# Kernel optimization log

Measured on AMD Instinct MI355X. Metric: run time of the kernel, lower is better.

Reference implementation:

```python
import jax, jax.numpy as jnp
import numpy as np

N_NODES = 100000
N_EDGES = 1000000
D_NODE = 64
D_EDGE = 32
D_OUT = 64
EPS = 1e-07
BETA = 1.0


def setup_inputs() -> dict:
    key = jax.random.key(0)
    ks = jax.random.split(key, 6)
    node_feats = jax.random.normal(ks[0], (N_NODES, D_NODE), dtype=jnp.float32)
    edge_feats = jax.random.normal(ks[1], (N_EDGES, D_EDGE), dtype=jnp.float32)
    src = jax.random.randint(ks[2], (N_EDGES,), 0, N_NODES, dtype=jnp.int32)
    dst = jax.random.randint(ks[3], (N_EDGES,), 0, N_NODES, dtype=jnp.int32)
    We = jax.random.normal(ks[4], (D_EDGE, D_OUT), dtype=jnp.float32) / np.sqrt(D_EDGE)
    be = jnp.zeros((D_OUT,), dtype=jnp.float32)
    Wm = jax.random.normal(ks[5], (D_NODE, D_OUT), dtype=jnp.float32) / np.sqrt(D_NODE)
    bm = jnp.zeros((D_OUT,), dtype=jnp.float32)
    return {"node_feats": node_feats, "edge_feats": edge_feats, "src": src,
            "dst": dst, "We": We, "be": be, "Wm": Wm, "bm": bm}


def reference(node_feats, edge_feats, src, dst, We, be, Wm, bm):
    n = node_feats.shape[0]
    # edge encoder + u_add_e: m_e = h_src + Linear(e)
    m = node_feats[src] + (edge_feats @ We + be)          # [E, D]
    m = jax.nn.relu(m) + EPS
    # segmented (per-destination) softmax over edges, per feature channel
    z = m * BETA
    zmax = jax.ops.segment_max(z, dst, num_segments=n)    # [N, D]
    ez = jnp.exp(z - zmax[dst])                           # [E, D]
    denom = jax.ops.segment_sum(ez, dst, num_segments=n)  # [N, D]
    a = ez / denom[dst]                                   # [E, D]
    # weighted scatter-sum aggregation
    agg = jax.ops.segment_sum(m * a, dst, num_segments=n) # [N, D]
    feats = node_feats + agg
    # mlp_layers=1 -> single Linear
    return feats @ Wm + bm
```

## Files before the change

kernel.cpp:

```cpp
#include <hip/hip_runtime.h>

#define D_NODE 64
#define D_EDGE 32
#define D_OUT  64
#define EPSF   1e-7f
#define CAP    48
#define CHUNK  8

typedef const __attribute__((address_space(1))) unsigned int guint_t;
typedef __attribute__((address_space(3))) unsigned int luint_t;

__global__ __launch_bounds__(256) void genconv_build_kernel(
    const int* __restrict__ src,
    const int* __restrict__ dst,
    int* __restrict__ cnt,
    int2* __restrict__ slots,
    int E)
{
    const int e = blockIdx.x * blockDim.x + threadIdx.x;
    if (e >= E) return;
    const int d = dst[e];
    const int pos = atomicAdd(&cnt[d], 1);
    if (pos < CAP)
        slots[d * CAP + pos] = make_int2(e, src[e]);
}

__global__ __launch_bounds__(256) void genconv_gather_kernel(
    const float* __restrict__ node,
    const float* __restrict__ ef,
    const int*  __restrict__ cnt,
    const int2* __restrict__ slots,
    const float* __restrict__ We,
    const float* __restrict__ be,
    const float* __restrict__ Wm,
    const float* __restrict__ bm,
    float* __restrict__ out,
    int N)
{
    __shared__ float wm_s[D_NODE * D_OUT];
    __shared__ __align__(16) float efs[4][2][CHUNK * D_EDGE];
    __shared__ __align__(16) float fbuf[4][D_NODE];

    for (int i = threadIdx.x; i < D_NODE * D_OUT; i += blockDim.x)
        wm_s[i] = Wm[i];
    __syncthreads();

    const int lane  = (int)(threadIdx.x & 63);
    const int wslot = (int)(threadIdx.x >> 6);
    float* const efA = efs[wslot][0];
    float* const efB = efs[wslot][1];

    float w[D_EDGE];
#pragma unroll
    for (int k = 0; k < D_EDGE; ++k)
        w[k] = We[k * D_OUT + lane];
    const float bias_e = be[lane];
    const float bias_m = bm[lane];

    const int wid = (int)((blockIdx.x * blockDim.x + threadIdx.x) >> 6);
    const int nw  = (int)((gridDim.x * blockDim.x) >> 6);

    int n = wid;
    int   c_pf   = 0;
    int2  sl_pf  = make_int2(0, 0);
    float res_pf = 0.0f;
    if (n < N) {
        c_pf   = cnt[n];
        sl_pf  = (lane < CAP) ? slots[n * CAP + lane] : make_int2(0, 0);
        res_pf = node[(size_t)n * D_NODE + lane];
    }

    struct HBank { float h0, h1, h2, h3, h4, h5, h6, h7; };

    while (n < N) {
        const int c = min(c_pf, CAP);
        const int e_l = (lane < c) ? sl_pf.x : 0;
        const int s_l = (lane < c) ? sl_pf.y : 0;
        const float fres = res_pf;

        const int n_next = n + nw;
        if (n_next < N) {
            c_pf   = cnt[n_next];
            sl_pf  = (lane < CAP) ? slots[n_next * CAP + lane] : make_int2(0, 0);
            res_pf = node[(size_t)n_next * D_NODE + lane];
        }
        __builtin_amdgcn_sched_barrier(0);

        float num = 0.0f, den = 0.0f;

        auto stage = [&](int base, float* dstLDS) {
            const int r  = base + (lane >> 3);
            const int er = __builtin_amdgcn_ds_bpermute(r << 2, e_l);
            const float* g = ef + (size_t)er * D_EDGE + ((lane & 7) << 2);
            __builtin_amdgcn_global_load_lds((guint_t*)g, (luint_t*)dstLDS, 16, 0, 0);
        };
        auto hload = [&](int base, HBank& H) {
            const int s0 = __builtin_amdgcn_readlane(s_l, base + 0);
            const int s1 = __builtin_amdgcn_readlane(s_l, base + 1);
            const int s2 = __builtin_amdgcn_readlane(s_l, base + 2);
            const int s3 = __builtin_amdgcn_readlane(s_l, base + 3);
            const int s4 = __builtin_amdgcn_readlane(s_l, base + 4);
            const int s5 = __builtin_amdgcn_readlane(s_l, base + 5);
            const int s6 = __builtin_amdgcn_readlane(s_l, base + 6);
            const int s7 = __builtin_amdgcn_readlane(s_l, base + 7);
            H.h0 = node[(size_t)s0 * D_NODE + lane];
            H.h1 = node[(size_t)s1 * D_NODE + lane];
            H.h2 = node[(size_t)s2 * D_NODE + lane];
            H.h3 = node[(size_t)s3 * D_NODE + lane];
            H.h4 = node[(size_t)s4 * D_NODE + lane];
            H.h5 = node[(size_t)s5 * D_NODE + lane];
            H.h6 = node[(size_t)s6 * D_NODE + lane];
            H.h7 = node[(size_t)s7 * D_NODE + lane];
        };
        auto pairop = [&](float ha, float hb, const float* eb0, bool second_ok) {
            const float* eb1 = eb0 + D_EDGE;
            float v0 = bias_e, v1 = bias_e;
#pragma unroll
            for (int k4 = 0; k4 < 8; ++k4) {
                const float4 a0 = *(const float4*)(eb0 + k4 * 4);
                const float4 a1 = *(const float4*)(eb1 + k4 * 4);
                v0 = fmaf(a0.x, w[4 * k4 + 0], v0);
                v0 = fmaf(a0.y, w[4 * k4 + 1], v0);
                v0 = fmaf(a0.z, w[4 * k4 + 2], v0);
                v0 = fmaf(a0.w, w[4 * k4 + 3], v0);
                v1 = fmaf(a1.x, w[4 * k4 + 0], v1);
                v1 = fmaf(a1.y, w[4 * k4 + 1], v1);
                v1 = fmaf(a1.z, w[4 * k4 + 2], v1);
                v1 = fmaf(a1.w, w[4 * k4 + 3], v1);
            }
            const float m0 = fmaxf(ha + v0, 0.0f) + EPSF;
            const float z0 = __expf(m0);
            num = fmaf(m0, z0, num);
            den += z0;
            if (second_ok) {
                const float m1 = fmaxf(hb + v1, 0.0f) + EPSF;
                const float z1 = __expf(m1);
                num = fmaf(m1, z1, num);
                den += z1;
            }
        };
        auto consume = [&](const float* eb, HBank& H, int base) {
            if (base + 0 < c) pairop(H.h0, H.h1, eb + 0 * D_EDGE, base + 1 < c);
            if (base + 2 < c) pairop(H.h2, H.h3, eb + 2 * D_EDGE, base + 3 < c);
            if (base + 4 < c) pairop(H.h4, H.h5, eb + 4 * D_EDGE, base + 5 < c);
            if (base + 6 < c) pairop(H.h6, H.h7, eb + 6 * D_EDGE, base + 7 < c);
        };

        const int nch = (c + CHUNK - 1) >> 3;
        if (nch > 0) {
            HBank HA, HB_;
            stage(0, efA);
            hload(0, HA);
            for (int p = 0; ; ) {
                {
                    const bool more = (p + 1 < nch);
                    if (more) { stage((p + 1) * CHUNK, efB); hload((p + 1) * CHUNK, HB_); }
                    if (more) asm volatile("s_waitcnt vmcnt(9)" ::: "memory");
                    else      asm volatile("s_waitcnt vmcnt(0)" ::: "memory");
                    __builtin_amdgcn_sched_barrier(0);
                    consume(efA, HA, p * CHUNK);
                    if (++p >= nch) break;
                }
                {
                    const bool more = (p + 1 < nch);
                    if (more) { stage((p + 1) * CHUNK, efA); hload((p + 1) * CHUNK, HA); }
                    if (more) asm volatile("s_waitcnt vmcnt(9)" ::: "memory");
                    else      asm volatile("s_waitcnt vmcnt(0)" ::: "memory");
                    __builtin_amdgcn_sched_barrier(0);
                    consume(efB, HB_, p * CHUNK);
                    if (++p >= nch) break;
                }
            }
        }

        float f = fres;
        if (c > 0)
            f += num / den;

        fbuf[wslot][lane] = f;
        float acc = bias_m;
#pragma unroll
        for (int d4 = 0; d4 < D_NODE / 4; ++d4) {
            const float4 fv = *(const float4*)&fbuf[wslot][d4 * 4];
            acc = fmaf(fv.x, wm_s[(d4 * 4 + 0) * D_OUT + lane], acc);
            acc = fmaf(fv.y, wm_s[(d4 * 4 + 1) * D_OUT + lane], acc);
            acc = fmaf(fv.z, wm_s[(d4 * 4 + 2) * D_OUT + lane], acc);
            acc = fmaf(fv.w, wm_s[(d4 * 4 + 3) * D_OUT + lane], acc);
        }
        out[(size_t)n * D_NODE + lane] = acc;

        n = n_next;
    }
}

extern "C" void kernel_launch(void* const* d_in, const int* in_sizes, int n_in,
                              void* d_out, int out_size, void* d_ws, size_t ws_size,
                              hipStream_t stream)
{
    const float* node = (const float*)d_in[0];
    const float* ef   = (const float*)d_in[1];
    const int*   src  = (const int*)d_in[2];
    const int*   dst  = (const int*)d_in[3];
    const float* We   = (const float*)d_in[4];
    const float* be   = (const float*)d_in[5];
    const float* Wm   = (const float*)d_in[6];
    const float* bm   = (const float*)d_in[7];
    float* out = (float*)d_out;

    const int N = in_sizes[0] / D_NODE;
    const int E = in_sizes[2];

    int*  cnt   = (int*)d_ws;
    int2* slots = (int2*)(cnt + N);

    hipMemsetAsync(cnt, 0, (size_t)N * sizeof(int), stream);

    genconv_build_kernel<<<(E + 255) / 256, 256, 0, stream>>>(src, dst, cnt, slots, E);

    genconv_gather_kernel<<<1536, 256, 0, stream>>>(node, ef, cnt, slots,
                                                    We, be, Wm, bm, out, N);
}
```

Baseline: 393.8 us.

## Fuse memset, build and gather into one cooperative kernel with dynamic node batches

Merges the counter reset, edge-bucketing build and the gather/softmax/MLP phase into a single cooperative kernel separated by grid-wide syncs, removing two extra launches and the memset. The gather phase also replaces static strided node assignment with per-slice atomic work counters that hand out batches of consecutive nodes, improving load balance and locality. It trades this for grid-sync cost, a grid limited to resident occupancy, and a fallback path with three launches if the cooperative launch fails.

```diff
diff --git a/kernel.cpp b/kernel.cpp
--- a/kernel.cpp
+++ b/kernel.cpp
@@ -1,4 +1,7 @@
 #include <hip/hip_runtime.h>
+#include <hip/hip_cooperative_groups.h>
+
+namespace cg = cooperative_groups;
 
 #define D_NODE 64
 #define D_EDGE 32
@@ -6,50 +9,34 @@
 #define EPSF   1e-7f
 #define CAP    48
 #define CHUNK  8
+#define NCTR   64
+#define BATCH  8
 
 typedef const __attribute__((address_space(1))) unsigned int guint_t;
 typedef __attribute__((address_space(3))) unsigned int luint_t;
 
-__global__ __launch_bounds__(256) void genconv_build_kernel(
-    const int* __restrict__ src,
-    const int* __restrict__ dst,
-    int* __restrict__ cnt,
-    int2* __restrict__ slots,
-    int E)
-{
-    const int e = blockIdx.x * blockDim.x + threadIdx.x;
-    if (e >= E) return;
-    const int d = dst[e];
-    const int pos = atomicAdd(&cnt[d], 1);
-    if (pos < CAP)
-        slots[d * CAP + pos] = make_int2(e, src[e]);
-}
-
-__global__ __launch_bounds__(256) void genconv_gather_kernel(
-    const float* __restrict__ node,
-    const float* __restrict__ ef,
-    const int*  __restrict__ cnt,
-    const int2* __restrict__ slots,
-    const float* __restrict__ We,
-    const float* __restrict__ be,
-    const float* __restrict__ Wm,
+__device__ __forceinline__ void build_phase(
+    const int* __restrict__ src, const int* __restrict__ dst,
+    int* __restrict__ cnt, int2* __restrict__ slots,
+    int E, int gtid, int gsz)
+{
+    for (int e = gtid; e < E; e += gsz) {
+        const int d = dst[e];
+        const int pos = atomicAdd(&cnt[d], 1);
+        if (pos < CAP)
+            slots[d * CAP + pos] = make_int2(e, src[e]);
+    }
+}
+
+__device__ __forceinline__ void gather_phase(
+    const float* __restrict__ node, const float* __restrict__ ef,
+    const int* __restrict__ cnt, const int2* __restrict__ slots,
+    int* __restrict__ ctrs,
+    const float* __restrict__ We, const float* __restrict__ be,
     const float* __restrict__ bm,
-    float* __restrict__ out,
-    int N)
-{
-    __shared__ float wm_s[D_NODE * D_OUT];
-    __shared__ __align__(16) float efs[4][2][CHUNK * D_EDGE];
-    __shared__ __align__(16) float fbuf[4][D_NODE];
-
-    for (int i = threadIdx.x; i < D_NODE * D_OUT; i += blockDim.x)
-        wm_s[i] = Wm[i];
-    __syncthreads();
-
-    const int lane  = (int)(threadIdx.x & 63);
-    const int wslot = (int)(threadIdx.x >> 6);
-    float* const efA = efs[wslot][0];
-    float* const efB = efs[wslot][1];
-
+    const float* wm_s, float* fbuf_w, float* efA, float* efB,
+    float* __restrict__ out, int N, int lane, int wid_g)
+{
     float w[D_EDGE];
 #pragma unroll
     for (int k = 0; k < D_EDGE; ++k)
@@ -57,14 +44,25 @@
     const float bias_e = be[lane];
     const float bias_m = bm[lane];
 
-    const int wid = (int)((blockIdx.x * blockDim.x + threadIdx.x) >> 6);
-    const int nw  = (int)((gridDim.x * blockDim.x) >> 6);
-
-    int n = wid;
+    const int slice   = wid_g & (NCTR - 1);
+    const int SLICE   = (N + NCTR - 1) / NCTR;
+    const int s_begin = slice * SLICE;
+    const int s_end   = min(s_begin + SLICE, N);
+
+    auto grab = [&]() -> int {
+        int g = 0;
+        if (lane == 0) g = atomicAdd(&ctrs[slice], BATCH);
+        return s_begin + __shfl(g, 0);
+    };
+
+    int n = grab();
+    int nextbase = grab();
+    int idx = 0;
+
     int   c_pf   = 0;
     int2  sl_pf  = make_int2(0, 0);
     float res_pf = 0.0f;
-    if (n < N) {
+    if (n < s_end) {
         c_pf   = cnt[n];
         sl_pf  = (lane < CAP) ? slots[n * CAP + lane] : make_int2(0, 0);
         res_pf = node[(size_t)n * D_NODE + lane];
@@ -72,14 +70,15 @@
 
     struct HBank { float h0, h1, h2, h3, h4, h5, h6, h7; };
 
-    while (n < N) {
+    while (n < s_end) {
         const int c = min(c_pf, CAP);
         const int e_l = (lane < c) ? sl_pf.x : 0;
         const int s_l = (lane < c) ? sl_pf.y : 0;
         const float fres = res_pf;
 
-        const int n_next = n + nw;
-        if (n_next < N) {
+        const bool roll  = (idx == BATCH - 1);
+        const int n_next = roll ? nextbase : (n + 1);
+        if (n_next < s_end) {
             c_pf   = cnt[n_next];
             sl_pf  = (lane < CAP) ? slots[n_next * CAP + lane] : make_int2(0, 0);
             res_pf = node[(size_t)n_next * D_NODE + lane];
@@ -177,11 +176,11 @@
         if (c > 0)
             f += num / den;
 
-        fbuf[wslot][lane] = f;
+        fbuf_w[lane] = f;
         float acc = bias_m;
 #pragma unroll
         for (int d4 = 0; d4 < D_NODE / 4; ++d4) {
-            const float4 fv = *(const float4*)&fbuf[wslot][d4 * 4];
+            const float4 fv = *(const float4*)&fbuf_w[d4 * 4];
             acc = fmaf(fv.x, wm_s[(d4 * 4 + 0) * D_OUT + lane], acc);
             acc = fmaf(fv.y, wm_s[(d4 * 4 + 1) * D_OUT + lane], acc);
             acc = fmaf(fv.z, wm_s[(d4 * 4 + 2) * D_OUT + lane], acc);
@@ -189,8 +188,78 @@
         }
         out[(size_t)n * D_NODE + lane] = acc;
 
+        if (roll) { idx = 0; nextbase = grab(); }
+        else      { ++idx; }
         n = n_next;
     }
+}
+
+__global__ __launch_bounds__(256) void genconv_fused_kernel(
+    const float* __restrict__ node, const float* __restrict__ ef,
+    const int* __restrict__ src, const int* __restrict__ dst,
+    int* __restrict__ cnt, int2* __restrict__ slots, int* __restrict__ ctrs,
+    const float* __restrict__ We, const float* __restrict__ be,
+    const float* __restrict__ Wm, const float* __restrict__ bm,
+    float* __restrict__ out, int N, int E)
+{
+    __shared__ float wm_s[D_NODE * D_OUT];
+    __shared__ __align__(16) float efs[4][2][CHUNK * D_EDGE];
+    __shared__ __align__(16) float fbuf[4][D_NODE];
+
+    const int gtid = (int)(blockIdx.x * blockDim.x + threadIdx.x);
+    const int gsz  = (int)(gridDim.x * blockDim.x);
+
+    for (int i = threadIdx.x; i < D_NODE * D_OUT; i += blockDim.x)
+        wm_s[i] = Wm[i];
+
+    for (int i = gtid; i < N; i += gsz) cnt[i] = 0;
+    if (gtid < NCTR) ctrs[gtid] = 0;
+
+    cg::this_grid().sync();
+
+    build_phase(src, dst, cnt, slots, E, gtid, gsz);
+
+    __threadfence();
+    cg::this_grid().sync();
+
+    const int lane  = (int)(threadIdx.x & 63);
+    const int wslot = (int)(threadIdx.x >> 6);
+    gather_phase(node, ef, cnt, slots, ctrs, We, be, bm,
+                 wm_s, fbuf[wslot], efs[wslot][0], efs[wslot][1],
+                 out, N, lane, gtid >> 6);
+}
+
+__global__ __launch_bounds__(256) void genconv_build_kernel(
+    const int* __restrict__ src, const int* __restrict__ dst,
+    int* __restrict__ cnt, int2* __restrict__ slots, int E)
+{
+    build_phase(src, dst, cnt, slots, E,
+                (int)(blockIdx.x * blockDim.x + threadIdx.x),
+                (int)(gridDim.x * blockDim.x));
+}
+
+__global__ __launch_bounds__(256) void genconv_gather_kernel(
+    const float* __restrict__ node, const float* __restrict__ ef,
+    const int* __restrict__ cnt, const int2* __restrict__ slots,
+    int* __restrict__ ctrs,
+    const float* __restrict__ We, const float* __restrict__ be,
+    const float* __restrict__ Wm, const float* __restrict__ bm,
+    float* __restrict__ out, int N)
+{
+    __shared__ float wm_s[D_NODE * D_OUT];
+    __shared__ __align__(16) float efs[4][2][CHUNK * D_EDGE];
+    __shared__ __align__(16) float fbuf[4][D_NODE];
+
+    for (int i = threadIdx.x; i < D_NODE * D_OUT; i += blockDim.x)
+        wm_s[i] = Wm[i];
+    __syncthreads();
+
+    const int lane  = (int)(threadIdx.x & 63);
+    const int wslot = (int)(threadIdx.x >> 6);
+    gather_phase(node, ef, cnt, slots, ctrs, We, be, bm,
+                 wm_s, fbuf[wslot], efs[wslot][0], efs[wslot][1],
+                 out, N, lane,
+                 (int)((blockIdx.x * blockDim.x + threadIdx.x) >> 6));
 }
 
 extern "C" void kernel_launch(void* const* d_in, const int* in_sizes, int n_in,
@@ -210,13 +279,39 @@
     const int N = in_sizes[0] / D_NODE;
     const int E = in_sizes[2];
 
-    int*  cnt   = (int*)d_ws;
+    int*  ctrs  = (int*)d_ws;
+    int*  cnt   = ctrs + NCTR;
     int2* slots = (int2*)(cnt + N);
 
-    hipMemsetAsync(cnt, 0, (size_t)N * sizeof(int), stream);
-
-    genconv_build_kernel<<<(E + 255) / 256, 256, 0, stream>>>(src, dst, cnt, slots, E);
-
-    genconv_gather_kernel<<<1536, 256, 0, stream>>>(node, ef, cnt, slots,
-                                                    We, be, Wm, bm, out, N);
-}
+    static int coop_grid = 0;
+    if (coop_grid == 0) {
+        int maxb = 0;
+        hipError_t oc = hipOccupancyMaxActiveBlocksPerMultiprocessor(
+            &maxb, (const void*)genconv_fused_kernel, 256, 0);
+        int ncu = 256;
+        hipDeviceProp_t prop;
+        int dev = 0;
+        if (hipGetDevice(&dev) == hipSuccess &&
+            hipGetDeviceProperties(&prop, dev) == hipSuccess)
+            ncu = prop.multiProcessorCount;
+        if (oc != hipSuccess || maxb <= 0) maxb = 4;
+        coop_grid = maxb * ncu;
+    }
+
+    void* kargs[] = {
+        (void*)&node, (void*)&ef, (void*)&src, (void*)&dst,
+        (void*)&cnt, (void*)&slots, (void*)&ctrs,
+        (void*)&We, (void*)&be, (void*)&Wm, (void*)&bm,
+        (void*)&out, (void*)&N, (void*)&E
+    };
+    hipError_t rc = hipLaunchCooperativeKernel(
+        (void*)genconv_fused_kernel, dim3(coop_grid), dim3(256),
+        kargs, 0, stream);
+
+    if (rc != hipSuccess) {
+        hipMemsetAsync(ctrs, 0, (size_t)(NCTR + N) * sizeof(int), stream);
+        genconv_build_kernel<<<(E + 255) / 256, 256, 0, stream>>>(src, dst, cnt, slots, E);
+        genconv_gather_kernel<<<2048, 256, 0, stream>>>(node, ef, cnt, slots, ctrs,
+                                                        We, be, Wm, bm, out, N);
+    }
+}
```

Result: slower. 633.3 us (+60.8%).

## Pipeline edge gathers across node boundaries with two-deep slot prefetch

Applied to the files above, without the earlier changes.

Restructures the per-wave gather loop into one continuous software pipeline. While the last chunk of the current node is consumed, the first chunk of edge features and source node rows for the next node is already being loaded, and slot lists are prefetched two nodes ahead. This removes the full vmcnt(0) drain at each node boundary. The grid also grows from 1536 to 2048 blocks. Costs are more live registers, more complex waitcnt bookkeeping with the vmcnt(13)/vmcnt(9) counts, and some redundant loads from clamped indices at the tail.

```diff
diff --git a/kernel.cpp b/kernel.cpp
--- a/kernel.cpp
+++ b/kernel.cpp
@@ -47,8 +47,9 @@
 
     const int lane  = (int)(threadIdx.x & 63);
     const int wslot = (int)(threadIdx.x >> 6);
-    float* const efA = efs[wslot][0];
-    float* const efB = efs[wslot][1];
+    float* const efA    = efs[wslot][0];
+    float* const efB    = efs[wslot][1];
+    float* const fbuf_w = fbuf[wslot];
 
     float w[D_EDGE];
 #pragma unroll
@@ -60,137 +61,146 @@
     const int wid = (int)((blockIdx.x * blockDim.x + threadIdx.x) >> 6);
     const int nw  = (int)((gridDim.x * blockDim.x) >> 6);
 
-    int n = wid;
-    int   c_pf   = 0;
-    int2  sl_pf  = make_int2(0, 0);
-    float res_pf = 0.0f;
-    if (n < N) {
-        c_pf   = cnt[n];
-        sl_pf  = (lane < CAP) ? slots[n * CAP + lane] : make_int2(0, 0);
-        res_pf = node[(size_t)n * D_NODE + lane];
+    int nCur = wid;
+    if (nCur >= N) return;
+
+    struct HBank { float h0, h1, h2, h3, h4, h5, h6, h7; };
+    HBank HA, HB_;
+
+    auto stage = [&](int base, int elanes, float* dstLDS) {
+        const int r  = base + (lane >> 3);
+        const int er = __builtin_amdgcn_ds_bpermute(r << 2, elanes);
+        const float* g = ef + (size_t)er * D_EDGE + ((lane & 7) << 2);
+        __builtin_amdgcn_global_load_lds((guint_t*)g, (luint_t*)dstLDS, 16, 0, 0);
+    };
+    auto hload = [&](int base, int slanes, HBank& H) {
+        const int s0 = __builtin_amdgcn_readlane(slanes, base + 0);
+        const int s1 = __builtin_amdgcn_readlane(slanes, base + 1);
+        const int s2 = __builtin_amdgcn_readlane(slanes, base + 2);
+        const int s3 = __builtin_amdgcn_readlane(slanes, base + 3);
+        const int s4 = __builtin_amdgcn_readlane(slanes, base + 4);
+        const int s5 = __builtin_amdgcn_readlane(slanes, base + 5);
+        const int s6 = __builtin_amdgcn_readlane(slanes, base + 6);
+        const int s7 = __builtin_amdgcn_readlane(slanes, base + 7);
+        H.h0 = node[(size_t)s0 * D_NODE + lane];
+        H.h1 = node[(size_t)s1 * D_NODE + lane];
+        H.h2 = node[(size_t)s2 * D_NODE + lane];
+        H.h3 = node[(size_t)s3 * D_NODE + lane];
+        H.h4 = node[(size_t)s4 * D_NODE + lane];
+        H.h5 = node[(size_t)s5 * D_NODE + lane];
+        H.h6 = node[(size_t)s6 * D_NODE + lane];
+        H.h7 = node[(size_t)s7 * D_NODE + lane];
+    };
+
+    float num = 0.0f, den = 0.0f;
+
+    auto pairop = [&](float ha, float hb, const float* eb0, bool second_ok) {
+        const float* eb1 = eb0 + D_EDGE;
+        float v0 = bias_e, v1 = bias_e;
+#pragma unroll
+        for (int k4 = 0; k4 < 8; ++k4) {
+            const float4 a0 = *(const float4*)(eb0 + k4 * 4);
+            const float4 a1 = *(const float4*)(eb1 + k4 * 4);
+            v0 = fmaf(a0.x, w[4 * k4 + 0], v0);
+            v0 = fmaf(a0.y, w[4 * k4 + 1], v0);
+            v0 = fmaf(a0.z, w[4 * k4 + 2], v0);
+            v0 = fmaf(a0.w, w[4 * k4 + 3], v0);
+            v1 = fmaf(a1.x, w[4 * k4 + 0], v1);
+            v1 = fmaf(a1.y, w[4 * k4 + 1], v1);
+            v1 = fmaf(a1.z, w[4 * k4 + 2], v1);
+            v1 = fmaf(a1.w, w[4 * k4 + 3], v1);
+        }
+        const float m0 = fmaxf(ha + v0, 0.0f) + EPSF;
+        const float z0 = __expf(m0);
+        num = fmaf(m0, z0, num);
+        den += z0;
+        if (second_ok) {
+            const float m1 = fmaxf(hb + v1, 0.0f) + EPSF;
+            const float z1 = __expf(m1);
+            num = fmaf(m1, z1, num);
+            den += z1;
+        }
+    };
+
+    int   rcC = cnt[nCur];
+    int2  cSL = (lane < CAP) ? slots[(size_t)nCur * CAP + lane] : make_int2(0, 0);
+    float cF  = node[(size_t)nCur * D_NODE + lane];
+    const int nid1 = min(nCur + nw, N - 1);
+    int  rxC = cnt[nid1];
+    int2 xSL = (lane < CAP) ? slots[(size_t)nid1 * CAP + lane] : make_int2(0, 0);
+    int cC = min(rcC, CAP);
+    int cE = (lane < cC) ? cSL.x : 0;
+    int cS = (lane < cC) ? cSL.y : 0;
+    stage(0, cE, efA);
+    hload(0, cS, HA);
+    int nC = min(rxC, CAP);
+    int nE = (lane < nC) ? xSL.x : 0;
+    int nS = (lane < nC) ? xSL.y : 0;
+    int nid2 = min(nCur + 2 * nw, N - 1);
+    int  rC  = cnt[nid2];
+    int2 rSL = (lane < CAP) ? slots[(size_t)nid2 * CAP + lane] : make_int2(0, 0);
+    __builtin_amdgcn_sched_barrier(0);
+
+    int  p     = 0;
+    bool first = true;
+    bool alive = true;
+
+#define STEP(EF_C, H_C, EF_S, H_S)                                            \
+    {                                                                          \
+        const int  nch   = (cC + CHUNK - 1) >> 3;                              \
+        const int  nch0  = (nch > 0) ? nch : 1;                                \
+        const bool lastc = (p == nch0 - 1);                                    \
+        if (!lastc) { stage((p + 1) * CHUNK, cE, EF_S); hload((p + 1) * CHUNK, cS, H_S); } \
+        else        { stage(0, nE, EF_S);               hload(0, nS, H_S); }   \
+        __builtin_amdgcn_sched_barrier(0);                                     \
+        if (first)        { asm volatile("s_waitcnt vmcnt(0)" ::: "memory"); first = false; } \
+        else if (p == 0)  { asm volatile("s_waitcnt vmcnt(13)" ::: "memory"); } \
+        else              { asm volatile("s_waitcnt vmcnt(9)" ::: "memory"); }  \
+        __builtin_amdgcn_sched_barrier(0);                                     \
+        {                                                                      \
+            const int base = p * CHUNK;                                        \
+            if (base + 0 < cC) pairop(H_C.h0, H_C.h1, EF_C + 0 * D_EDGE, base + 1 < cC); \
+            if (base + 2 < cC) pairop(H_C.h2, H_C.h3, EF_C + 2 * D_EDGE, base + 3 < cC); \
+            if (base + 4 < cC) pairop(H_C.h4, H_C.h5, EF_C + 4 * D_EDGE, base + 5 < cC); \
+            if (base + 6 < cC) pairop(H_C.h6, H_C.h7, EF_C + 6 * D_EDGE, base + 7 < cC); \
+        }                                                                      \
+        if (lastc) {                                                           \
+            float f = cF;                                                      \
+            if (cC > 0) f += num / den;                                        \
+            fbuf_w[lane] = f;                                                  \
+            float acc = bias_m;                                                \
+            _Pragma("unroll")                                                  \
+            for (int d4 = 0; d4 < D_NODE / 4; ++d4) {                          \
+                const float4 fv = *(const float4*)&fbuf_w[d4 * 4];             \
+                acc = fmaf(fv.x, wm_s[(d4 * 4 + 0) * D_OUT + lane], acc);      \
+                acc = fmaf(fv.y, wm_s[(d4 * 4 + 1) * D_OUT + lane], acc);      \
+                acc = fmaf(fv.z, wm_s[(d4 * 4 + 2) * D_OUT + lane], acc);      \
+                acc = fmaf(fv.w, wm_s[(d4 * 4 + 3) * D_OUT + lane], acc);      \
+            }                                                                  \
+            out[(size_t)nCur * D_NODE + lane] = acc;              \
+            nCur += nw;                                                        \
+            if (nCur >= N) { alive = false; }                                  \
+            else {                                                             \
+                cC = nC; cE = nE; cS = nS; p = 0; num = 0.0f; den = 0.0f;      \
+                cF = node[(size_t)nCur * D_NODE + lane];          \
+                nC = min(rC, CAP);                                             \
+                nE = (lane < nC) ? rSL.x : 0;                                  \
+                nS = (lane < nC) ? rSL.y : 0;                                  \
+                nid2 = min(nCur + 2 * nw, N - 1);                              \
+                rC  = cnt[nid2];                                  \
+                rSL = (lane < CAP) ? slots[(size_t)nid2 * CAP + lane]          \
+                                   : make_int2(0, 0);             \
+                __builtin_amdgcn_sched_barrier(0);                             \
+            }                                                                  \
+        } else { ++p; }                                                        \
     }
 
-    struct HBank { float h0, h1, h2, h3, h4, h5, h6, h7; };
-
-    while (n < N) {
-        const int c = min(c_pf, CAP);
-        const int e_l = (lane < c) ? sl_pf.x : 0;
-        const int s_l = (lane < c) ? sl_pf.y : 0;
-        const float fres = res_pf;
-
-        const int n_next = n + nw;
-        if (n_next < N) {
-            c_pf   = cnt[n_next];
-            sl_pf  = (lane < CAP) ? slots[n_next * CAP + lane] : make_int2(0, 0);
-            res_pf = node[(size_t)n_next * D_NODE + lane];
-        }
-        __builtin_amdgcn_sched_barrier(0);
-
-        float num = 0.0f, den = 0.0f;
-
-        auto stage = [&](int base, float* dstLDS) {
-            const int r  = base + (lane >> 3);
-            const int er = __builtin_amdgcn_ds_bpermute(r << 2, e_l);
-            const float* g = ef + (size_t)er * D_EDGE + ((lane & 7) << 2);
-            __builtin_amdgcn_global_load_lds((guint_t*)g, (luint_t*)dstLDS, 16, 0, 0);
-        };
-        auto hload = [&](int base, HBank& H) {
-            const int s0 = __builtin_amdgcn_readlane(s_l, base + 0);
-            const int s1 = __builtin_amdgcn_readlane(s_l, base + 1);
-            const int s2 = __builtin_amdgcn_readlane(s_l, base + 2);
-            const int s3 = __builtin_amdgcn_readlane(s_l, base + 3);
-            const int s4 = __builtin_amdgcn_readlane(s_l, base + 4);
-            const int s5 = __builtin_amdgcn_readlane(s_l, base + 5);
-            const int s6 = __builtin_amdgcn_readlane(s_l, base + 6);
-            const int s7 = __builtin_amdgcn_readlane(s_l, base + 7);
-            H.h0 = node[(size_t)s0 * D_NODE + lane];
-            H.h1 = node[(size_t)s1 * D_NODE + lane];
-            H.h2 = node[(size_t)s2 * D_NODE + lane];
-            H.h3 = node[(size_t)s3 * D_NODE + lane];
-            H.h4 = node[(size_t)s4 * D_NODE + lane];
-            H.h5 = node[(size_t)s5 * D_NODE + lane];
-            H.h6 = node[(size_t)s6 * D_NODE + lane];
-            H.h7 = node[(size_t)s7 * D_NODE + lane];
-        };
-        auto pairop = [&](float ha, float hb, const float* eb0, bool second_ok) {
-            const float* eb1 = eb0 + D_EDGE;
-            float v0 = bias_e, v1 = bias_e;
-#pragma unroll
-            for (int k4 = 0; k4 < 8; ++k4) {
-                const float4 a0 = *(const float4*)(eb0 + k4 * 4);
-                const float4 a1 = *(const float4*)(eb1 + k4 * 4);
-                v0 = fmaf(a0.x, w[4 * k4 + 0], v0);
-                v0 = fmaf(a0.y, w[4 * k4 + 1], v0);
-                v0 = fmaf(a0.z, w[4 * k4 + 2], v0);
-                v0 = fmaf(a0.w, w[4 * k4 + 3], v0);
-                v1 = fmaf(a1.x, w[4 * k4 + 0], v1);
-                v1 = fmaf(a1.y, w[4 * k4 + 1], v1);
-                v1 = fmaf(a1.z, w[4 * k4 + 2], v1);
-                v1 = fmaf(a1.w, w[4 * k4 + 3], v1);
-            }
-            const float m0 = fmaxf(ha + v0, 0.0f) + EPSF;
-            const float z0 = __expf(m0);
-            num = fmaf(m0, z0, num);
-            den += z0;
-            if (second_ok) {
-                const float m1 = fmaxf(hb + v1, 0.0f) + EPSF;
-                const float z1 = __expf(m1);
-                num = fmaf(m1, z1, num);
-                den += z1;
-            }
-        };
-        auto consume = [&](const float* eb, HBank& H, int base) {
-            if (base + 0 < c) pairop(H.h0, H.h1, eb + 0 * D_EDGE, base + 1 < c);
-            if (base + 2 < c) pairop(H.h2, H.h3, eb + 2 * D_EDGE, base + 3 < c);
-            if (base + 4 < c) pairop(H.h4, H.h5, eb + 4 * D_EDGE, base + 5 < c);
-            if (base + 6 < c) pairop(H.h6, H.h7, eb + 6 * D_EDGE, base + 7 < c);
-        };
-
-        const int nch = (c + CHUNK - 1) >> 3;
-        if (nch > 0) {
-            HBank HA, HB_;
-            stage(0, efA);
-            hload(0, HA);
-            for (int p = 0; ; ) {
-                {
-                    const bool more = (p + 1 < nch);
-                    if (more) { stage((p + 1) * CHUNK, efB); hload((p + 1) * CHUNK, HB_); }
-                    if (more) asm volatile("s_waitcnt vmcnt(9)" ::: "memory");
-                    else      asm volatile("s_waitcnt vmcnt(0)" ::: "memory");
-                    __builtin_amdgcn_sched_barrier(0);
-                    consume(efA, HA, p * CHUNK);
-                    if (++p >= nch) break;
-                }
-                {
-                    const bool more = (p + 1 < nch);
-                    if (more) { stage((p + 1) * CHUNK, efA); hload((p + 1) * CHUNK, HA); }
-                    if (more) asm volatile("s_waitcnt vmcnt(9)" ::: "memory");
-                    else      asm volatile("s_waitcnt vmcnt(0)" ::: "memory");
-                    __builtin_amdgcn_sched_barrier(0);
-                    consume(efB, HB_, p * CHUNK);
-                    if (++p >= nch) break;
-                }
-            }
-        }
-
-        float f = fres;
-        if (c > 0)
-            f += num / den;
-
-        fbuf[wslot][lane] = f;
-        float acc = bias_m;
-#pragma unroll
-        for (int d4 = 0; d4 < D_NODE / 4; ++d4) {
-            const float4 fv = *(const float4*)&fbuf[wslot][d4 * 4];
-            acc = fmaf(fv.x, wm_s[(d4 * 4 + 0) * D_OUT + lane], acc);
-            acc = fmaf(fv.y, wm_s[(d4 * 4 + 1) * D_OUT + lane], acc);
-            acc = fmaf(fv.z, wm_s[(d4 * 4 + 2) * D_OUT + lane], acc);
-            acc = fmaf(fv.w, wm_s[(d4 * 4 + 3) * D_OUT + lane], acc);
-        }
-        out[(size_t)n * D_NODE + lane] = acc;
-
-        n = n_next;
+    while (alive) {
+        STEP(efA, HA, efB, HB_)
+        if (!alive) break;
+        STEP(efB, HB_, efA, HA)
     }
+#undef STEP
 }
 
 extern "C" void kernel_launch(void* const* d_in, const int* in_sizes, int n_in,
@@ -217,6 +227,6 @@
 
     genconv_build_kernel<<<(E + 255) / 256, 256, 0, stream>>>(src, dst, cnt, slots, E);
 
-    genconv_gather_kernel<<<1536, 256, 0, stream>>>(node, ef, cnt, slots,
+    genconv_gather_kernel<<<2048, 256, 0, stream>>>(node, ef, cnt, slots,
                                                     We, be, Wm, bm, out, N);
 }
```

New measurement: 388.4 us. Within noise of the previous version (-1.4%).
